# Optimization experiments

Measured on AMD Instinct MI355X. Metric: run time of the kernel, lower is better.

## Reference

```python
import jax, jax.numpy as jnp
import numpy as np

B, N, A = 4096, 16, 8          # envs, num_agents, num_actions
D_IN, H1, DP, DZ = 128, 64, 64, 64  # obs dim, gnn hidden, obs_proc dim, gat fc dim


def _init(k, shape):
    return jax.random.normal(k, shape, jnp.float32) / np.sqrt(shape[0]).astype(np.float32)


def setup_inputs() -> dict:
    key = jax.random.key(0)
    ks = jax.random.split(key, 8)
    return {
        "obs": jax.random.normal(ks[0], (B * N, D_IN), jnp.float32),
        "policies": jax.random.uniform(ks[1], (B * N, A), dtype=jnp.float32),
        "actions": jax.random.uniform(ks[2], (B * N, A), dtype=jnp.float32),
        "W1": _init(ks[3], (D_IN, H1)), "b1": jnp.zeros((H1,), jnp.float32),
        "W2": _init(ks[4], (H1, DP)), "b2": jnp.zeros((DP,), jnp.float32),
        "Wfc": _init(ks[5], (DP, DZ)),
        "Wattn": _init(ks[6], (2 * DZ, 1)),
        "Wv": _init(ks[7], (DP + A, 1)), "bv": jnp.zeros((1,), jnp.float32),
    }


def reference(obs, policies, actions, W1, b1, W2, b2, Wfc, Wattn, Wv, bv):
    obs = obs.reshape(B, N, D_IN)
    # --- CriticInputPreprocess: two mean-aggregation GNN layers on a complete
    # graph with self-loops -> every node sees the per-env mean.
    agg1 = jnp.mean(obs, axis=1)                      # [B, D_IN]
    h = jax.nn.relu(agg1 @ W1 + b1)                   # [B, H1] (identical across nodes)
    obs_proc1 = h @ W2 + b2                           # mean of identical features is itself
    obs_proc = jnp.broadcast_to(obs_proc1[:, None, :], (B, N, DP))  # [B, N, DP]
    # --- GATLayer edge attention: e_{d<-s} = leaky_relu(attn([z_s, z_d]))
    z_ = obs_proc @ Wfc                               # [B, N, DZ]
    a_src = (z_ @ Wattn[:DZ]).squeeze(-1)             # [B, N]
    a_dst = (z_ @ Wattn[DZ:]).squeeze(-1)             # [B, N]
    e = jax.nn.leaky_relu(a_src[:, None, :] + a_dst[:, :, None])    # [B, dst, src]
    w = jax.nn.sigmoid(e)                             # [B, N, N]
    pi = policies.reshape(B, N, A)
    act = actions.reshape(B, N, A)
    # mailbox mix per (dst d, src k): z = w*act_k + (1-w)*pi_k
    z = w[..., None] * act[:, None, :, :] + (1.0 - w[..., None]) * pi[:, None, :, :]  # [B,d,k,A]
    # place_policies/place_zs + mean over src axis collapses to:
    # y[b,d,j] = (pi[b,j] + sum_{k!=j} z[b,d,k]) / N
    y = (jnp.sum(z, axis=2, keepdims=True) - z + pi[:, None, :, :]) / N               # [B,d,j,A]
    obs_rep = jnp.broadcast_to(obs_proc[:, None, :, :], (B, N, N, DP))                # obs_proc[b, j]
    obs_final = jnp.concatenate([obs_rep, y], axis=-1).reshape(B * N, N, DP + A)
    x = obs_final @ Wv + bv                           # [B*N, N, 1]
    return x, w.reshape(B * N, N, 1)
```

## Files before the change

### kernel.cpp

```cpp
#include <hip/hip_runtime.h>

#define BB   4096
#define NN   16
#define AA   8
#define DIN  128
#define H1C  64
#define DPC  64
#define DZC  64

#define GENV 8
#define NTHR 512


__device__ __forceinline__ float lane_bcast(float v, int lane) {
    return __int_as_float(__builtin_amdgcn_readlane(__float_as_int(v), lane));
}

__global__ __launch_bounds__(NTHR, 4)
void critic_kernel(const float* __restrict__ obs,
                   const float* __restrict__ policies,
                   const float* __restrict__ actions,
                   const float* __restrict__ W1,
                   const float* __restrict__ b1,
                   const float* __restrict__ W2,
                   const float* __restrict__ b2,
                   const float* __restrict__ Wfc,
                   const float* __restrict__ Wattn,
                   const float* __restrict__ Wv,
                   const float* __restrict__ bv,
                   float* __restrict__ out_x,
                   float* __restrict__ out_w)
{
    __shared__ float4 sW1T4[H1C * 32];
    __shared__ float sV1[H1C];
    __shared__ float sV2[H1C];
    __shared__ float sS[2];
    __shared__ float sDv[GENV][16];
    __shared__ float sWsum[DZC];
    __shared__ float sWv64[DPC];
    __shared__ float sU[DPC];

    const int tid = threadIdx.x;
    const int l   = tid & 63;
    const int w   = tid >> 6;
    const int e   = blockIdx.x * GENV + w;

    {
        const int c   = tid & 63;
        const int grp = tid >> 6;
        #pragma unroll
        for (int i = 0; i < 4; ++i) {
            const int d0 = 4 * (i * 8 + grp);
            const float w0  = W1[(d0 + 0) * H1C + c];
            const float w1_ = W1[(d0 + 1) * H1C + c];
            const float w2_ = W1[(d0 + 2) * H1C + c];
            const float w3_ = W1[(d0 + 3) * H1C + c];
            sW1T4[c * 32 + ((d0 >> 2) ^ (c & 7))] = make_float4(w0, w1_, w2_, w3_);
        }
    }

    const float2* o2p = reinterpret_cast<const float2*>(obs) + (size_t)e * (NN * DIN / 2);
    float2 ov[NN];
    #pragma unroll
    for (int r = 0; r < NN; ++r) ov[r] = o2p[r * 64 + l];

    const float* Pb = policies + (size_t)e * (NN * AA);
    const float* Ab = actions  + (size_t)e * (NN * AA);
    const float pv0 = Pb[l], pv1 = Pb[64 + l];
    const float av0 = Ab[l], av1 = Ab[64 + l];

    const float b1v = b1[l];
    const float va  = Wv[64 + (l & 7)];
    const float bvv = bv[0];

    if (w == 7) {
        const float b2v  = b2[l];
        const float wsum = Wattn[l] + Wattn[DZC + l];
        const float wvv  = Wv[l];
        sWsum[l] = wsum;
        sWv64[l] = wvv;

        float u = 0.0f;
        {
            const float4* WfcR = reinterpret_cast<const float4*>(Wfc) + (size_t)l * (DZC / 4);
            const float4* ws4  = reinterpret_cast<const float4*>(sWsum);
            #pragma unroll
            for (int j4 = 0; j4 < DZC / 4; ++j4) {
                const float4 wq = WfcR[j4];
                const float4 s  = ws4[j4];
                u = fmaf(wq.x, s.x, u); u = fmaf(wq.y, s.y, u);
                u = fmaf(wq.z, s.z, u); u = fmaf(wq.w, s.w, u);
            }
        }
        sU[l] = u;
        float v1 = 0.0f, v2 = 0.0f;
        {
            const float4* W2R = reinterpret_cast<const float4*>(W2) + (size_t)l * (DPC / 4);
            const float4* su4 = reinterpret_cast<const float4*>(sU);
            const float4* sv4 = reinterpret_cast<const float4*>(sWv64);
            #pragma unroll
            for (int j4 = 0; j4 < DPC / 4; ++j4) {
                const float4 wq = W2R[j4];
                const float4 a  = su4[j4];
                const float4 b  = sv4[j4];
                v1 = fmaf(wq.x, a.x, v1); v1 = fmaf(wq.y, a.y, v1);
                v1 = fmaf(wq.z, a.z, v1); v1 = fmaf(wq.w, a.w, v1);
                v2 = fmaf(wq.x, b.x, v2); v2 = fmaf(wq.y, b.y, v2);
                v2 = fmaf(wq.z, b.z, v2); v2 = fmaf(wq.w, b.w, v2);
            }
        }
        float tb2u = b2v * u;
        float tb2w = b2v * wvv;
        #pragma unroll
        for (int m = 32; m >= 1; m >>= 1) {
            tb2u += __shfl_xor(tb2u, m);
            tb2w += __shfl_xor(tb2w, m);
        }
        sV1[l] = v1;
        sV2[l] = v2;
        if (l == 0) { sS[0] = tb2u; sS[1] = tb2w; }
    }

    float ax, ay;
    {
        float sx = 0.0f, sy = 0.0f;
        #pragma unroll
        for (int r = 0; r < NN; ++r) { sx += ov[r].x; sy += ov[r].y; }
        const float inv = 1.0f / 16.0f;
        ax = sx * inv;
        ay = sy * inv;
    }

    float q0 = (pv0 - av0) * va;
    float q1 = (pv1 - av1) * va;
    float fq = q0 + q1;
    float fp = (pv0 + pv1) * va;
    #pragma unroll
    for (int m = 1; m <= 4; m <<= 1) {
        q0 += __shfl_xor(q0, m);
        q1 += __shfl_xor(q1, m);
    }
    #pragma unroll
    for (int m = 32; m >= 1; m >>= 1) {
        fq += __shfl_xor(fq, m);
        fp += __shfl_xor(fp, m);
    }
    if ((l & 7) == 0) {
        sDv[w][l >> 3]       = q0;
        sDv[w][8 + (l >> 3)] = q1;
    }

    __syncthreads();

    float a0 = b1v, a1 = 0.0f, a2 = 0.0f, a3 = 0.0f;
    #pragma unroll
    for (int d4 = 0; d4 < DIN / 4; ++d4) {
        const float4 w4 = sW1T4[l * 32 + (d4 ^ (l & 7))];
        a0 = fmaf(lane_bcast(ax, 2 * d4),     w4.x, a0);
        a1 = fmaf(lane_bcast(ay, 2 * d4),     w4.y, a1);
        a2 = fmaf(lane_bcast(ax, 2 * d4 + 1), w4.z, a2);
        a3 = fmaf(lane_bcast(ay, 2 * d4 + 1), w4.w, a3);
    }
    const float h = fmaxf((a0 + a1) + (a2 + a3), 0.0f);

    const float v1l  = sV1[l];
    const float v2l  = sV2[l];
    const float tb2u = sS[0];
    const float tb2w = sS[1];

    float t0 = h * v1l;
    float t1 = h * v2l;
    #pragma unroll
    for (int m = 32; m >= 1; m >>= 1) {
        t0 += __shfl_xor(t0, m);
        t1 += __shfl_xor(t1, m);
    }
    const float logit = t0 + tb2u;
    const float eV  = (logit > 0.0f) ? logit : 0.01f * logit;
    const float wgt = 1.0f / (1.0f + expf(-eV));
    const float c   = t1 + tb2w + bvv;
    const float Sv  = fp - wgt * fq;

    const float invN = 1.0f / 16.0f;
    const int j0 = (4 * l) & 15;
    float4 xo, wo;
    xo.x = fmaf(wgt, sDv[w][j0 + 0], Sv) * invN + c;
    xo.y = fmaf(wgt, sDv[w][j0 + 1], Sv) * invN + c;
    xo.z = fmaf(wgt, sDv[w][j0 + 2], Sv) * invN + c;
    xo.w = fmaf(wgt, sDv[w][j0 + 3], Sv) * invN + c;
    wo.x = wo.y = wo.z = wo.w = wgt;

    const size_t base = (size_t)e * (NN * NN) + 4 * l;
    *reinterpret_cast<float4*>(out_x + base) = xo;
    *reinterpret_cast<float4*>(out_w + base) = wo;
}

extern "C" void kernel_launch(void* const* d_in, const int* in_sizes, int n_in,
                              void* d_out, int out_size, void* d_ws, size_t ws_size,
                              hipStream_t stream) {
    const float* obs      = (const float*)d_in[0];
    const float* policies = (const float*)d_in[1];
    const float* actions  = (const float*)d_in[2];
    const float* W1       = (const float*)d_in[3];
    const float* b1       = (const float*)d_in[4];
    const float* W2       = (const float*)d_in[5];
    const float* b2       = (const float*)d_in[6];
    const float* Wfc      = (const float*)d_in[7];
    const float* Wattn    = (const float*)d_in[8];
    const float* Wv       = (const float*)d_in[9];
    const float* bv       = (const float*)d_in[10];

    float* out_x = (float*)d_out;
    float* out_w = out_x + (size_t)BB * NN * NN;

    critic_kernel<<<BB / GENV, NTHR, 0, stream>>>(obs, policies, actions,
                                                  W1, b1, W2, b2, Wfc, Wattn, Wv, bv,
                                                  out_x, out_w);
}
```

Measured before the change: 17.42 us.

## Process two environments per wavefront to amortize per-block W1 staging

Each wavefront now handles two environments instead of one, so each block covers 16 envs and the shared-memory W1 transpose and the weight-derived vectors are built once per 16 envs rather than once per 8. Obs loads switch to float4 with a cross-half shuffle for the mean, and the second env's obs load is issued after the barrier to overlap with compute. The aim is to cut redundant per-block setup work and halve the block count. In exchange the grid shrinks to 256 blocks with lower occupancy (launch bounds 2) and higher register pressure, which could reduce latency hiding.

```diff
diff --git a/kernel.cpp b/kernel.cpp
--- a/kernel.cpp
+++ b/kernel.cpp
@@ -8,7 +8,8 @@
 #define DPC  64
 #define DZC  64
 
-#define GENV 8
+#define GENV 16
+#define WENV 2
 #define NTHR 512
 
 
@@ -16,7 +17,7 @@
     return __int_as_float(__builtin_amdgcn_readlane(__float_as_int(v), lane));
 }
 
-__global__ __launch_bounds__(NTHR, 4)
+__global__ __launch_bounds__(NTHR, 2)
 void critic_kernel(const float* __restrict__ obs,
                    const float* __restrict__ policies,
                    const float* __restrict__ actions,
@@ -43,7 +44,10 @@
     const int tid = threadIdx.x;
     const int l   = tid & 63;
     const int w   = tid >> 6;
-    const int e   = blockIdx.x * GENV + w;
+    const int leA = 2 * w;
+    const int leB = 2 * w + 1;
+    const int eA  = blockIdx.x * GENV + leA;
+    const int eB  = blockIdx.x * GENV + leB;
 
     {
         const int c   = tid & 63;
@@ -59,15 +63,21 @@
         }
     }
 
-    const float2* o2p = reinterpret_cast<const float2*>(obs) + (size_t)e * (NN * DIN / 2);
-    float2 ov[NN];
-    #pragma unroll
-    for (int r = 0; r < NN; ++r) ov[r] = o2p[r * 64 + l];
-
-    const float* Pb = policies + (size_t)e * (NN * AA);
-    const float* Ab = actions  + (size_t)e * (NN * AA);
-    const float pv0 = Pb[l], pv1 = Pb[64 + l];
-    const float av0 = Ab[l], av1 = Ab[64 + l];
+    const float4* o4A = reinterpret_cast<const float4*>(obs + (size_t)eA * NN * DIN);
+    const float4* o4B = reinterpret_cast<const float4*>(obs + (size_t)eB * NN * DIN);
+    float4 ovA[8];
+    #pragma unroll
+    for (int t = 0; t < 8; ++t) ovA[t] = o4A[t * 64 + l];
+
+    float pv0[WENV], pv1[WENV], av0[WENV], av1[WENV];
+    {
+        const float* PbA = policies + (size_t)eA * (NN * AA);
+        const float* AbA = actions  + (size_t)eA * (NN * AA);
+        const float* PbB = policies + (size_t)eB * (NN * AA);
+        const float* AbB = actions  + (size_t)eB * (NN * AA);
+        pv0[0] = PbA[l]; pv1[0] = PbA[64 + l]; av0[0] = AbA[l]; av1[0] = AbA[64 + l];
+        pv0[1] = PbB[l]; pv1[1] = PbB[64 + l]; av0[1] = AbB[l]; av1[1] = AbB[64 + l];
+    }
 
     const float b1v = b1[l];
     const float va  = Wv[64 + (l & 7)];
@@ -121,78 +131,99 @@
         if (l == 0) { sS[0] = tb2u; sS[1] = tb2w; }
     }
 
-    float ax, ay;
-    {
-        float sx = 0.0f, sy = 0.0f;
-        #pragma unroll
-        for (int r = 0; r < NN; ++r) { sx += ov[r].x; sy += ov[r].y; }
-        const float inv = 1.0f / 16.0f;
-        ax = sx * inv;
-        ay = sy * inv;
-    }
-
-    float q0 = (pv0 - av0) * va;
-    float q1 = (pv1 - av1) * va;
-    float fq = q0 + q1;
-    float fp = (pv0 + pv1) * va;
-    #pragma unroll
-    for (int m = 1; m <= 4; m <<= 1) {
-        q0 += __shfl_xor(q0, m);
-        q1 += __shfl_xor(q1, m);
-    }
-    #pragma unroll
-    for (int m = 32; m >= 1; m >>= 1) {
-        fq += __shfl_xor(fq, m);
-        fp += __shfl_xor(fp, m);
-    }
-    if ((l & 7) == 0) {
-        sDv[w][l >> 3]       = q0;
-        sDv[w][8 + (l >> 3)] = q1;
+    float fqv[WENV], fpv[WENV];
+    #pragma unroll
+    for (int ee = 0; ee < WENV; ++ee) {
+        float q0 = (pv0[ee] - av0[ee]) * va;
+        float q1 = (pv1[ee] - av1[ee]) * va;
+        float fq = q0 + q1;
+        float fp = (pv0[ee] + pv1[ee]) * va;
+        #pragma unroll
+        for (int m = 1; m <= 4; m <<= 1) {
+            q0 += __shfl_xor(q0, m);
+            q1 += __shfl_xor(q1, m);
+        }
+        #pragma unroll
+        for (int m = 32; m >= 1; m >>= 1) {
+            fq += __shfl_xor(fq, m);
+            fp += __shfl_xor(fp, m);
+        }
+        fqv[ee] = fq;
+        fpv[ee] = fp;
+        const int le = leA + ee;
+        if ((l & 7) == 0) {
+            sDv[le][l >> 3]       = q0;
+            sDv[le][8 + (l >> 3)] = q1;
+        }
     }
 
     __syncthreads();
 
-    float a0 = b1v, a1 = 0.0f, a2 = 0.0f, a3 = 0.0f;
-    #pragma unroll
-    for (int d4 = 0; d4 < DIN / 4; ++d4) {
-        const float4 w4 = sW1T4[l * 32 + (d4 ^ (l & 7))];
-        a0 = fmaf(lane_bcast(ax, 2 * d4),     w4.x, a0);
-        a1 = fmaf(lane_bcast(ay, 2 * d4),     w4.y, a1);
-        a2 = fmaf(lane_bcast(ax, 2 * d4 + 1), w4.z, a2);
-        a3 = fmaf(lane_bcast(ay, 2 * d4 + 1), w4.w, a3);
-    }
-    const float h = fmaxf((a0 + a1) + (a2 + a3), 0.0f);
+    float4 ovB[8];
+    #pragma unroll
+    for (int t = 0; t < 8; ++t) ovB[t] = o4B[t * 64 + l];
 
     const float v1l  = sV1[l];
     const float v2l  = sV2[l];
     const float tb2u = sS[0];
     const float tb2w = sS[1];
-
-    float t0 = h * v1l;
-    float t1 = h * v2l;
-    #pragma unroll
-    for (int m = 32; m >= 1; m >>= 1) {
-        t0 += __shfl_xor(t0, m);
-        t1 += __shfl_xor(t1, m);
-    }
-    const float logit = t0 + tb2u;
-    const float eV  = (logit > 0.0f) ? logit : 0.01f * logit;
-    const float wgt = 1.0f / (1.0f + expf(-eV));
-    const float c   = t1 + tb2w + bvv;
-    const float Sv  = fp - wgt * fq;
-
     const float invN = 1.0f / 16.0f;
-    const int j0 = (4 * l) & 15;
-    float4 xo, wo;
-    xo.x = fmaf(wgt, sDv[w][j0 + 0], Sv) * invN + c;
-    xo.y = fmaf(wgt, sDv[w][j0 + 1], Sv) * invN + c;
-    xo.z = fmaf(wgt, sDv[w][j0 + 2], Sv) * invN + c;
-    xo.w = fmaf(wgt, sDv[w][j0 + 3], Sv) * invN + c;
-    wo.x = wo.y = wo.z = wo.w = wgt;
-
-    const size_t base = (size_t)e * (NN * NN) + 4 * l;
-    *reinterpret_cast<float4*>(out_x + base) = xo;
-    *reinterpret_cast<float4*>(out_w + base) = wo;
+    const int   j0   = (4 * l) & 15;
+
+    #pragma unroll
+    for (int ee = 0; ee < WENV; ++ee) {
+        const int le = leA + ee;
+        float4* ov = (ee == 0) ? ovA : ovB;
+
+        float4 ag;
+        {
+            float4 a = make_float4(0.f, 0.f, 0.f, 0.f);
+            #pragma unroll
+            for (int t = 0; t < 8; ++t) {
+                a.x += ov[t].x; a.y += ov[t].y; a.z += ov[t].z; a.w += ov[t].w;
+            }
+            a.x += __shfl_xor(a.x, 32);
+            a.y += __shfl_xor(a.y, 32);
+            a.z += __shfl_xor(a.z, 32);
+            a.w += __shfl_xor(a.w, 32);
+            ag = make_float4(a.x * invN, a.y * invN, a.z * invN, a.w * invN);
+        }
+
+        float a0 = b1v, a1 = 0.0f, a2 = 0.0f, a3 = 0.0f;
+        #pragma unroll
+        for (int d4 = 0; d4 < DIN / 4; ++d4) {
+            const float4 w4 = sW1T4[l * 32 + (d4 ^ (l & 7))];
+            a0 = fmaf(lane_bcast(ag.x, d4), w4.x, a0);
+            a1 = fmaf(lane_bcast(ag.y, d4), w4.y, a1);
+            a2 = fmaf(lane_bcast(ag.z, d4), w4.z, a2);
+            a3 = fmaf(lane_bcast(ag.w, d4), w4.w, a3);
+        }
+        const float h = fmaxf((a0 + a1) + (a2 + a3), 0.0f);
+
+        float t0 = h * v1l;
+        float t1 = h * v2l;
+        #pragma unroll
+        for (int m = 32; m >= 1; m >>= 1) {
+            t0 += __shfl_xor(t0, m);
+            t1 += __shfl_xor(t1, m);
+        }
+        const float logit = t0 + tb2u;
+        const float eV  = (logit > 0.0f) ? logit : 0.01f * logit;
+        const float wgt = 1.0f / (1.0f + expf(-eV));
+        const float c   = t1 + tb2w + bvv;
+        const float Sv  = fpv[ee] - wgt * fqv[ee];
+
+        float4 xo, wo;
+        xo.x = fmaf(wgt, sDv[le][j0 + 0], Sv) * invN + c;
+        xo.y = fmaf(wgt, sDv[le][j0 + 1], Sv) * invN + c;
+        xo.z = fmaf(wgt, sDv[le][j0 + 2], Sv) * invN + c;
+        xo.w = fmaf(wgt, sDv[le][j0 + 3], Sv) * invN + c;
+        wo.x = wo.y = wo.z = wo.w = wgt;
+
+        const size_t base = (size_t)(blockIdx.x * GENV + le) * (NN * NN) + 4 * l;
+        *reinterpret_cast<float4*>(out_x + base) = xo;
+        *reinterpret_cast<float4*>(out_w + base) = wo;
+    }
 }
 
 extern "C" void kernel_launch(void* const* d_in, const int* in_sizes, int n_in,
```

After: 18.96 us. +8.8%, slower.

## Process two environments per wavefront with software-pipelined obs loads

Applied to the files above, without the earlier changes.

The block shrinks to 256 threads while still covering 8 environments, so each wavefront now handles two environments. The second environment's obs rows are loaded while the first environment's hidden-layer matmul and outputs are computed. The W1 transpose into shared memory is also amortized over more environments per thread. The cost is higher register pressure from the second set of obs values, and fewer waves in flight to hide memory latency.

```diff
diff --git a/kernel.cpp b/kernel.cpp
--- a/kernel.cpp
+++ b/kernel.cpp
@@ -9,7 +9,7 @@
 #define DZC  64
 
 #define GENV 8
-#define NTHR 512
+#define NTHR 256
 
 
 __device__ __forceinline__ float lane_bcast(float v, int lane) {
@@ -43,37 +43,41 @@
     const int tid = threadIdx.x;
     const int l   = tid & 63;
     const int w   = tid >> 6;
-    const int e   = blockIdx.x * GENV + w;
-
-    {
-        const int c   = tid & 63;
-        const int grp = tid >> 6;
-        #pragma unroll
-        for (int i = 0; i < 4; ++i) {
-            const int d0 = 4 * (i * 8 + grp);
-            const float w0  = W1[(d0 + 0) * H1C + c];
-            const float w1_ = W1[(d0 + 1) * H1C + c];
-            const float w2_ = W1[(d0 + 2) * H1C + c];
-            const float w3_ = W1[(d0 + 3) * H1C + c];
-            sW1T4[c * 32 + ((d0 >> 2) ^ (c & 7))] = make_float4(w0, w1_, w2_, w3_);
-        }
-    }
-
-    const float2* o2p = reinterpret_cast<const float2*>(obs) + (size_t)e * (NN * DIN / 2);
-    float2 ov[NN];
+    const int leA = 2 * w;
+    const int leB = 2 * w + 1;
+    const int eA  = blockIdx.x * GENV + leA;
+    const int eB  = blockIdx.x * GENV + leB;
+
+    const float2* oA = reinterpret_cast<const float2*>(obs) + (size_t)eA * (NN * DIN / 2);
+    const float2* oB = reinterpret_cast<const float2*>(obs) + (size_t)eB * (NN * DIN / 2);
+    float2 ovA[NN];
     #pragma unroll
-    for (int r = 0; r < NN; ++r) ov[r] = o2p[r * 64 + l];
-
-    const float* Pb = policies + (size_t)e * (NN * AA);
-    const float* Ab = actions  + (size_t)e * (NN * AA);
-    const float pv0 = Pb[l], pv1 = Pb[64 + l];
-    const float av0 = Ab[l], av1 = Ab[64 + l];
+    for (int r = 0; r < NN; ++r) ovA[r] = oA[r * 64 + l];
+
+    {
+        #pragma unroll
+        for (int i = 0; i < 8; ++i) {
+            const int d0 = 4 * (i * 4 + w);
+            const float w0  = W1[(d0 + 0) * H1C + l];
+            const float w1_ = W1[(d0 + 1) * H1C + l];
+            const float w2_ = W1[(d0 + 2) * H1C + l];
+            const float w3_ = W1[(d0 + 3) * H1C + l];
+            sW1T4[l * 32 + ((d0 >> 2) ^ (l & 7))] = make_float4(w0, w1_, w2_, w3_);
+        }
+    }
+
+    const float* PbA = policies + (size_t)eA * (NN * AA);
+    const float* AbA = actions  + (size_t)eA * (NN * AA);
+    const float* PbB = policies + (size_t)eB * (NN * AA);
+    const float* AbB = actions  + (size_t)eB * (NN * AA);
+    const float pv0A = PbA[l], pv1A = PbA[64 + l], av0A = AbA[l], av1A = AbA[64 + l];
+    const float pv0B = PbB[l], pv1B = PbB[64 + l], av0B = AbB[l], av1B = AbB[64 + l];
 
     const float b1v = b1[l];
     const float va  = Wv[64 + (l & 7)];
     const float bvv = bv[0];
 
-    if (w == 7) {
+    if (w == 3) {
         const float b2v  = b2[l];
         const float wsum = Wattn[l] + Wattn[DZC + l];
         const float wvv  = Wv[l];
@@ -109,90 +113,111 @@
                 v2 = fmaf(wq.z, b.z, v2); v2 = fmaf(wq.w, b.w, v2);
             }
         }
-        float tb2u = b2v * u;
-        float tb2w = b2v * wvv;
+        float tb2u_ = b2v * u;
+        float tb2w_ = b2v * wvv;
         #pragma unroll
         for (int m = 32; m >= 1; m >>= 1) {
-            tb2u += __shfl_xor(tb2u, m);
-            tb2w += __shfl_xor(tb2w, m);
+            tb2u_ += __shfl_xor(tb2u_, m);
+            tb2w_ += __shfl_xor(tb2w_, m);
         }
         sV1[l] = v1;
         sV2[l] = v2;
-        if (l == 0) { sS[0] = tb2u; sS[1] = tb2w; }
-    }
-
-    float ax, ay;
-    {
-        float sx = 0.0f, sy = 0.0f;
-        #pragma unroll
-        for (int r = 0; r < NN; ++r) { sx += ov[r].x; sy += ov[r].y; }
-        const float inv = 1.0f / 16.0f;
-        ax = sx * inv;
-        ay = sy * inv;
-    }
-
-    float q0 = (pv0 - av0) * va;
-    float q1 = (pv1 - av1) * va;
-    float fq = q0 + q1;
-    float fp = (pv0 + pv1) * va;
-    #pragma unroll
-    for (int m = 1; m <= 4; m <<= 1) {
-        q0 += __shfl_xor(q0, m);
-        q1 += __shfl_xor(q1, m);
-    }
-    #pragma unroll
-    for (int m = 32; m >= 1; m >>= 1) {
-        fq += __shfl_xor(fq, m);
-        fp += __shfl_xor(fp, m);
-    }
-    if ((l & 7) == 0) {
-        sDv[w][l >> 3]       = q0;
-        sDv[w][8 + (l >> 3)] = q1;
+        if (l == 0) { sS[0] = tb2u_; sS[1] = tb2w_; }
+    }
+
+    float fqA, fpA, fqB, fpB;
+    {
+        float q0 = (pv0A - av0A) * va;
+        float q1 = (pv1A - av1A) * va;
+        float fq = q0 + q1;
+        float fp = (pv0A + pv1A) * va;
+        #pragma unroll
+        for (int m = 1; m <= 4; m <<= 1) { q0 += __shfl_xor(q0, m); q1 += __shfl_xor(q1, m); }
+        #pragma unroll
+        for (int m = 32; m >= 1; m >>= 1) { fq += __shfl_xor(fq, m); fp += __shfl_xor(fp, m); }
+        fqA = fq; fpA = fp;
+        if ((l & 7) == 0) { sDv[leA][l >> 3] = q0; sDv[leA][8 + (l >> 3)] = q1; }
+    }
+    {
+        float q0 = (pv0B - av0B) * va;
+        float q1 = (pv1B - av1B) * va;
+        float fq = q0 + q1;
+        float fp = (pv0B + pv1B) * va;
+        #pragma unroll
+        for (int m = 1; m <= 4; m <<= 1) { q0 += __shfl_xor(q0, m); q1 += __shfl_xor(q1, m); }
+        #pragma unroll
+        for (int m = 32; m >= 1; m >>= 1) { fq += __shfl_xor(fq, m); fp += __shfl_xor(fp, m); }
+        fqB = fq; fpB = fp;
+        if ((l & 7) == 0) { sDv[leB][l >> 3] = q0; sDv[leB][8 + (l >> 3)] = q1; }
     }
 
     __syncthreads();
-
-    float a0 = b1v, a1 = 0.0f, a2 = 0.0f, a3 = 0.0f;
-    #pragma unroll
-    for (int d4 = 0; d4 < DIN / 4; ++d4) {
-        const float4 w4 = sW1T4[l * 32 + (d4 ^ (l & 7))];
-        a0 = fmaf(lane_bcast(ax, 2 * d4),     w4.x, a0);
-        a1 = fmaf(lane_bcast(ay, 2 * d4),     w4.y, a1);
-        a2 = fmaf(lane_bcast(ax, 2 * d4 + 1), w4.z, a2);
-        a3 = fmaf(lane_bcast(ay, 2 * d4 + 1), w4.w, a3);
-    }
-    const float h = fmaxf((a0 + a1) + (a2 + a3), 0.0f);
 
     const float v1l  = sV1[l];
     const float v2l  = sV2[l];
     const float tb2u = sS[0];
     const float tb2w = sS[1];
-
-    float t0 = h * v1l;
-    float t1 = h * v2l;
+    const float invN = 1.0f / 16.0f;
+    const int   j0   = (4 * l) & 15;
+
+    auto process_env = [&](float ax, float ay, float fq, float fp, int le, int e) {
+        float a0 = b1v, a1 = 0.0f, a2 = 0.0f, a3 = 0.0f;
+        #pragma unroll
+        for (int d4 = 0; d4 < DIN / 4; ++d4) {
+            const float4 w4 = sW1T4[l * 32 + (d4 ^ (l & 7))];
+            a0 = fmaf(lane_bcast(ax, 2 * d4),     w4.x, a0);
+            a1 = fmaf(lane_bcast(ay, 2 * d4),     w4.y, a1);
+            a2 = fmaf(lane_bcast(ax, 2 * d4 + 1), w4.z, a2);
+            a3 = fmaf(lane_bcast(ay, 2 * d4 + 1), w4.w, a3);
+        }
+        const float h = fmaxf((a0 + a1) + (a2 + a3), 0.0f);
+
+        float t0 = h * v1l;
+        float t1 = h * v2l;
+        #pragma unroll
+        for (int m = 32; m >= 1; m >>= 1) { t0 += __shfl_xor(t0, m); t1 += __shfl_xor(t1, m); }
+        const float logit = t0 + tb2u;
+        const float eV  = (logit > 0.0f) ? logit : 0.01f * logit;
+        const float wgt = 1.0f / (1.0f + expf(-eV));
+        const float c   = t1 + tb2w + bvv;
+        const float Sv  = fp - wgt * fq;
+
+        float4 xo, wo;
+        xo.x = fmaf(wgt, sDv[le][j0 + 0], Sv) * invN + c;
+        xo.y = fmaf(wgt, sDv[le][j0 + 1], Sv) * invN + c;
+        xo.z = fmaf(wgt, sDv[le][j0 + 2], Sv) * invN + c;
+        xo.w = fmaf(wgt, sDv[le][j0 + 3], Sv) * invN + c;
+        wo.x = wo.y = wo.z = wo.w = wgt;
+
+        const size_t base = (size_t)e * (NN * NN) + 4 * l;
+        *reinterpret_cast<float4*>(out_x + base) = xo;
+        *reinterpret_cast<float4*>(out_w + base) = wo;
+    };
+
+    float axA, ayA;
+    {
+        float sx = 0.0f, sy = 0.0f;
+        #pragma unroll
+        for (int r = 0; r < NN; ++r) { sx += ovA[r].x; sy += ovA[r].y; }
+        axA = sx * invN;
+        ayA = sy * invN;
+    }
+
+    float2 ovB[NN];
     #pragma unroll
-    for (int m = 32; m >= 1; m >>= 1) {
-        t0 += __shfl_xor(t0, m);
-        t1 += __shfl_xor(t1, m);
-    }
-    const float logit = t0 + tb2u;
-    const float eV  = (logit > 0.0f) ? logit : 0.01f * logit;
-    const float wgt = 1.0f / (1.0f + expf(-eV));
-    const float c   = t1 + tb2w + bvv;
-    const float Sv  = fp - wgt * fq;
-
-    const float invN = 1.0f / 16.0f;
-    const int j0 = (4 * l) & 15;
-    float4 xo, wo;
-    xo.x = fmaf(wgt, sDv[w][j0 + 0], Sv) * invN + c;
-    xo.y = fmaf(wgt, sDv[w][j0 + 1], Sv) * invN + c;
-    xo.z = fmaf(wgt, sDv[w][j0 + 2], Sv) * invN + c;
-    xo.w = fmaf(wgt, sDv[w][j0 + 3], Sv) * invN + c;
-    wo.x = wo.y = wo.z = wo.w = wgt;
-
-    const size_t base = (size_t)e * (NN * NN) + 4 * l;
-    *reinterpret_cast<float4*>(out_x + base) = xo;
-    *reinterpret_cast<float4*>(out_w + base) = wo;
+    for (int r = 0; r < NN; ++r) ovB[r] = oB[r * 64 + l];
+
+    process_env(axA, ayA, fqA, fpA, leA, eA);
+
+    float axB, ayB;
+    {
+        float sx = 0.0f, sy = 0.0f;
+        #pragma unroll
+        for (int r = 0; r < NN; ++r) { sx += ovB[r].x; sy += ovB[r].y; }
+        axB = sx * invN;
+        ayB = sy * invN;
+    }
+    process_env(axB, ayB, fqB, fpB, leB, eB);
 }
 
 extern "C" void kernel_launch(void* const* d_in, const int* in_sizes, int n_in,
```

Result: slower. 35.26 us (+102.4%).

## Halve block size and load obs as float4 with cross-half lane reduction

Applied to the files above, without the earlier changes.

Block size drops from 8 environments (512 threads) to 4 environments (256 threads), so each block restages W1 into shared memory for fewer environments but more blocks run. Observation rows are now read as 8 float4 loads per lane instead of 16 float2 loads, and the two half-wave partial sums are combined with a shuffle-xor 32. The W1 contraction then broadcasts one lane per 4-element chunk. The obs loads are issued before the W1 staging to overlap latency, at the cost of twice as many blocks each repeating the W1 transpose.

```diff
diff --git a/kernel.cpp b/kernel.cpp
--- a/kernel.cpp
+++ b/kernel.cpp
@@ -8,8 +8,8 @@
 #define DPC  64
 #define DZC  64
 
-#define GENV 8
-#define NTHR 512
+#define GENV 4
+#define NTHR 256
 
 
 __device__ __forceinline__ float lane_bcast(float v, int lane) {
@@ -45,24 +45,22 @@
     const int w   = tid >> 6;
     const int e   = blockIdx.x * GENV + w;
 
+    const float4* o4 = reinterpret_cast<const float4*>(obs + (size_t)e * NN * DIN);
+    float4 ov[8];
+    #pragma unroll
+    for (int t = 0; t < 8; ++t) ov[t] = o4[t * 64 + l];
+
     {
-        const int c   = tid & 63;
-        const int grp = tid >> 6;
-        #pragma unroll
-        for (int i = 0; i < 4; ++i) {
-            const int d0 = 4 * (i * 8 + grp);
-            const float w0  = W1[(d0 + 0) * H1C + c];
-            const float w1_ = W1[(d0 + 1) * H1C + c];
-            const float w2_ = W1[(d0 + 2) * H1C + c];
-            const float w3_ = W1[(d0 + 3) * H1C + c];
-            sW1T4[c * 32 + ((d0 >> 2) ^ (c & 7))] = make_float4(w0, w1_, w2_, w3_);
-        }
-    }
-
-    const float2* o2p = reinterpret_cast<const float2*>(obs) + (size_t)e * (NN * DIN / 2);
-    float2 ov[NN];
-    #pragma unroll
-    for (int r = 0; r < NN; ++r) ov[r] = o2p[r * 64 + l];
+        #pragma unroll
+        for (int i = 0; i < 8; ++i) {
+            const int d0 = 4 * (i * 4 + w);
+            const float w0  = W1[(d0 + 0) * H1C + l];
+            const float w1_ = W1[(d0 + 1) * H1C + l];
+            const float w2_ = W1[(d0 + 2) * H1C + l];
+            const float w3_ = W1[(d0 + 3) * H1C + l];
+            sW1T4[l * 32 + ((d0 >> 2) ^ (l & 7))] = make_float4(w0, w1_, w2_, w3_);
+        }
+    }
 
     const float* Pb = policies + (size_t)e * (NN * AA);
     const float* Ab = actions  + (size_t)e * (NN * AA);
@@ -73,7 +71,7 @@
     const float va  = Wv[64 + (l & 7)];
     const float bvv = bv[0];
 
-    if (w == 7) {
+    if (w == 3) {
         const float b2v  = b2[l];
         const float wsum = Wattn[l] + Wattn[DZC + l];
         const float wvv  = Wv[l];
@@ -109,45 +107,45 @@
                 v2 = fmaf(wq.z, b.z, v2); v2 = fmaf(wq.w, b.w, v2);
             }
         }
-        float tb2u = b2v * u;
-        float tb2w = b2v * wvv;
+        float tb2u_ = b2v * u;
+        float tb2w_ = b2v * wvv;
         #pragma unroll
         for (int m = 32; m >= 1; m >>= 1) {
-            tb2u += __shfl_xor(tb2u, m);
-            tb2w += __shfl_xor(tb2w, m);
+            tb2u_ += __shfl_xor(tb2u_, m);
+            tb2w_ += __shfl_xor(tb2w_, m);
         }
         sV1[l] = v1;
         sV2[l] = v2;
-        if (l == 0) { sS[0] = tb2u; sS[1] = tb2w; }
-    }
-
-    float ax, ay;
+        if (l == 0) { sS[0] = tb2u_; sS[1] = tb2w_; }
+    }
+
+    float fqv, fpv;
     {
-        float sx = 0.0f, sy = 0.0f;
-        #pragma unroll
-        for (int r = 0; r < NN; ++r) { sx += ov[r].x; sy += ov[r].y; }
+        float q0 = (pv0 - av0) * va;
+        float q1 = (pv1 - av1) * va;
+        float fq = q0 + q1;
+        float fp = (pv0 + pv1) * va;
+        #pragma unroll
+        for (int m = 1; m <= 4; m <<= 1) { q0 += __shfl_xor(q0, m); q1 += __shfl_xor(q1, m); }
+        #pragma unroll
+        for (int m = 32; m >= 1; m >>= 1) { fq += __shfl_xor(fq, m); fp += __shfl_xor(fp, m); }
+        fqv = fq; fpv = fp;
+        if ((l & 7) == 0) { sDv[w][l >> 3] = q0; sDv[w][8 + (l >> 3)] = q1; }
+    }
+
+    float4 ag;
+    {
+        float4 a = make_float4(0.f, 0.f, 0.f, 0.f);
+        #pragma unroll
+        for (int t = 0; t < 8; ++t) {
+            a.x += ov[t].x; a.y += ov[t].y; a.z += ov[t].z; a.w += ov[t].w;
+        }
+        a.x += __shfl_xor(a.x, 32);
+        a.y += __shfl_xor(a.y, 32);
+        a.z += __shfl_xor(a.z, 32);
+        a.w += __shfl_xor(a.w, 32);
         const float inv = 1.0f / 16.0f;
-        ax = sx * inv;
-        ay = sy * inv;
-    }
-
-    float q0 = (pv0 - av0) * va;
-    float q1 = (pv1 - av1) * va;
-    float fq = q0 + q1;
-    float fp = (pv0 + pv1) * va;
-    #pragma unroll
-    for (int m = 1; m <= 4; m <<= 1) {
-        q0 += __shfl_xor(q0, m);
-        q1 += __shfl_xor(q1, m);
-    }
-    #pragma unroll
-    for (int m = 32; m >= 1; m >>= 1) {
-        fq += __shfl_xor(fq, m);
-        fp += __shfl_xor(fp, m);
-    }
-    if ((l & 7) == 0) {
-        sDv[w][l >> 3]       = q0;
-        sDv[w][8 + (l >> 3)] = q1;
+        ag = make_float4(a.x * inv, a.y * inv, a.z * inv, a.w * inv);
     }
 
     __syncthreads();
@@ -156,10 +154,10 @@
     #pragma unroll
     for (int d4 = 0; d4 < DIN / 4; ++d4) {
         const float4 w4 = sW1T4[l * 32 + (d4 ^ (l & 7))];
-        a0 = fmaf(lane_bcast(ax, 2 * d4),     w4.x, a0);
-        a1 = fmaf(lane_bcast(ay, 2 * d4),     w4.y, a1);
-        a2 = fmaf(lane_bcast(ax, 2 * d4 + 1), w4.z, a2);
-        a3 = fmaf(lane_bcast(ay, 2 * d4 + 1), w4.w, a3);
+        a0 = fmaf(lane_bcast(ag.x, d4), w4.x, a0);
+        a1 = fmaf(lane_bcast(ag.y, d4), w4.y, a1);
+        a2 = fmaf(lane_bcast(ag.z, d4), w4.z, a2);
+        a3 = fmaf(lane_bcast(ag.w, d4), w4.w, a3);
     }
     const float h = fmaxf((a0 + a1) + (a2 + a3), 0.0f);
 
@@ -179,7 +177,7 @@
     const float eV  = (logit > 0.0f) ? logit : 0.01f * logit;
     const float wgt = 1.0f / (1.0f + expf(-eV));
     const float c   = t1 + tb2w + bvv;
-    const float Sv  = fp - wgt * fq;
+    const float Sv  = fpv - wgt * fqv;
 
     const float invN = 1.0f / 16.0f;
     const int j0 = (4 * l) & 15;
```

Measured after the change: 19.23 us. +10.4%, slower.
